# Kernel optimization log

Measured on AMD Instinct MI355X. Metric: run time of the kernel, lower is better.

Reference implementation:

```python
import jax, jax.numpy as jnp
import numpy as np

N, E, G, D = 100000, 1600000, 1000, 32
EPS = 1e-5


def setup_inputs() -> dict:
    key = jax.random.key(0)
    ks = jax.random.split(key, 24)
    inp = {
        'h': jax.random.normal(ks[0], (N, D), dtype=jnp.float32),
        'src': jax.random.randint(ks[1], (E,), 0, N, dtype=jnp.int32),
        'dst': jax.random.randint(ks[2], (E,), 0, N, dtype=jnp.int32),
        'graph_id': jnp.sort(jax.random.randint(ks[3], (N,), 0, G, dtype=jnp.int32)),
    }
    dims = [D, 32, 32, 32, 1]
    ki = 4
    for i in range(4):
        inp[f'conv_w{i}'] = jax.random.normal(ks[ki], (dims[i], dims[i + 1]), dtype=jnp.float32) * 0.1; ki += 1
        inp[f'conv_b{i}'] = jax.random.normal(ks[ki], (dims[i + 1],), dtype=jnp.float32) * 0.1; ki += 1
        inp[f'bn_g{i}'] = jnp.ones((dims[i + 1],), dtype=jnp.float32)
        inp[f'bn_b{i}'] = jnp.zeros((dims[i + 1],), dtype=jnp.float32)
    mlp_dims = [D + 32 + 32 + 32 + 1, 128, 64, 1]  # 129 -> 128 -> 64 -> 1
    for i in range(3):
        inp[f'mlp_w{i}'] = jax.random.normal(ks[ki], (mlp_dims[i], mlp_dims[i + 1]), dtype=jnp.float32) * 0.1; ki += 1
        inp[f'mlp_b{i}'] = jax.random.normal(ks[ki], (mlp_dims[i + 1],), dtype=jnp.float32) * 0.1; ki += 1
    return inp


def _mean_agg(x, src, dst):
    # DGL update_all(copy_u, mean): h'_v = mean of h_u over in-neighbors u of v
    deg = jax.ops.segment_sum(jnp.ones((src.shape[0],), x.dtype), dst, num_segments=N)
    agg = jax.ops.segment_sum(x[src], dst, num_segments=N)
    return agg / jnp.maximum(deg, 1.0)[:, None]


def _bn(x, g, b):
    # BatchNorm1d in training mode: batch statistics over node dim
    m = x.mean(axis=0)
    v = x.var(axis=0)
    return g * (x - m) * jax.lax.rsqrt(v + EPS) + b


def reference(h, src, dst, graph_id,
              conv_w0, conv_b0, conv_w1, conv_b1, conv_w2, conv_b2, conv_w3, conv_b3,
              bn_g0, bn_b0, bn_g1, bn_b1, bn_g2, bn_b2, bn_g3, bn_b3,
              mlp_w0, mlp_b0, mlp_w1, mlp_b1, mlp_w2, mlp_b2):
    conv = [(conv_w0, conv_b0), (conv_w1, conv_b1), (conv_w2, conv_b2), (conv_w3, conv_b3)]
    bn = [(bn_g0, bn_b0), (bn_g1, bn_b1), (bn_g2, bn_b2), (bn_g3, bn_b3)]
    h_list = [h]
    x = h
    for (w, b), (g, bb) in zip(conv, bn):
        x = _mean_agg(x, src, dst) @ w + b      # GCNConv
        x = jax.nn.relu(_bn(x, g, bb))           # BN + ReLU
        h_list.append(x)
    h_final = jnp.concatenate(h_list, axis=1)    # [N, 129]
    # dgl.mean_nodes: per-graph mean pool
    cnt = jax.ops.segment_sum(jnp.ones((N,), h_final.dtype), graph_id, num_segments=G)
    hg = jax.ops.segment_sum(h_final, graph_id, num_segments=G) / jnp.maximum(cnt, 1.0)[:, None]
    hg = jax.nn.relu(hg @ mlp_w0 + mlp_b0)
    hg = jax.nn.relu(hg @ mlp_w1 + mlp_b1)
    hg = hg @ mlp_w2 + mlp_b2
    return hg.reshape(-1)                         # [G]
```

## Files before the change

### kernel.cpp

```cpp
#include <hip/hip_runtime.h>

#define NSLOT 32
#define BN_EPS 1e-5f
#define NSB 256
#define BKBITS 8
#define BKN 256
#define MAXBUCK 512

static inline int cdiv_h(int a, int b) { return (a + b - 1) / b; }

__device__ __forceinline__ float4 f4add(float4 a, float4 b) {
    return make_float4(a.x + b.x, a.y + b.y, a.z + b.z, a.w + b.w);
}

__device__ __forceinline__ unsigned bf16rtn(float x) {
    unsigned u = __float_as_uint(x);
    return (u + 0x7FFFu + ((u >> 16) & 1u)) >> 16;
}
__device__ __forceinline__ unsigned bf16pack2(float lo, float hi) {
    return bf16rtn(lo) | (bf16rtn(hi) << 16);
}
__device__ __forceinline__ float bfLO(unsigned u) { return __uint_as_float(u << 16); }
__device__ __forceinline__ float bfHI(unsigned u) { return __uint_as_float(u & 0xFFFF0000u); }

__device__ __forceinline__ int blk_excl_scan256(int v, int t) {
    __shared__ int wsum[4];
    int l = t & 63, w = t >> 6;
    int incl = v;
#pragma unroll
    for (int off = 1; off < 64; off <<= 1) {
        int o = __shfl_up(incl, off, 64);
        if (l >= off) incl += o;
    }
    if (l == 63) wsum[w] = incl;
    __syncthreads();
    int wofs = 0;
#pragma unroll
    for (int i = 0; i < 4; i++) wofs += (i < w) ? wsum[i] : 0;
    __syncthreads();
    return wofs + incl - v;
}

__device__ __forceinline__ int blk_excl_scan512(int v, int t) {
    __shared__ int wsum8[8];
    int l = t & 63, w = t >> 6;
    int incl = v;
#pragma unroll
    for (int off = 1; off < 64; off <<= 1) {
        int o = __shfl_up(incl, off, 64);
        if (l >= off) incl += o;
    }
    if (l == 63) wsum8[w] = incl;
    __syncthreads();
    int wofs = 0;
#pragma unroll
    for (int i = 0; i < 8; i++) wofs += (i < w) ? wsum8[i] : 0;
    __syncthreads();
    return wofs + incl - v;
}

__device__ __forceinline__ void bn_coef(const float* __restrict__ sSum, const float* __restrict__ sSq,
                                        const float* __restrict__ bg, const float* __restrict__ bb,
                                        float invN, int ch, float* aOut, float* cOut) {
    float S = 0.f, Q = 0.f;
#pragma unroll
    for (int s = 0; s < NSLOT; s++) { S += sSum[s * 32 + ch]; Q += sSq[s * 32 + ch]; }
    float m = S * invN;
    float var = Q * invN - m * m;
    if (var < 0.f) var = 0.f;
    float iv = rsqrtf(var + BN_EPS);
    float a = bg[ch] * iv;
    *aOut = a;
    *cOut = bb[ch] - m * a;
}


__global__ __launch_bounds__(256) void k_hist(const int* __restrict__ dst, int* __restrict__ histT,
                                              float* __restrict__ sSum, float* __restrict__ sSq,
                                              int E, int nbuck, int chunk) {
    __shared__ int bins[MAXBUCK];
    int k = blockIdx.x, t = threadIdx.x;
    if (k == 0) {
        for (int i = t; i < 4 * NSLOT * 32; i += 256) { sSum[i] = 0.f; sSq[i] = 0.f; }
    }
    for (int b = t; b < nbuck; b += 256) bins[b] = 0;
    __syncthreads();
    int lo = k * chunk, hi = lo + chunk; if (hi > E) hi = E;
    for (int i = lo + t; i < hi; i += 256) atomicAdd(&bins[dst[i] >> BKBITS], 1);
    __syncthreads();
    for (int b = t; b < nbuck; b += 256) histT[k * nbuck + b] = bins[b];
}


__global__ __launch_bounds__(256) void k_scanA(const int* __restrict__ histT, int* __restrict__ prefixB,
                                               int* __restrict__ totalP, int* __restrict__ totalU,
                                               const int* __restrict__ gid, int* __restrict__ gstart,
                                               int nbuck, int N, int G) {
    int b = blockIdx.x, k = threadIdx.x;
    int i = b * 256 + k;
    if (i < N) {
        int g = gid[i];
        int gp = (i == 0) ? -1 : gid[i - 1];
        for (int x = gp + 1; x <= g; ++x) gstart[x] = i;
        if (i == N - 1) { for (int x = g + 1; x <= G; ++x) gstart[x] = N; }
    }
    int c = histT[k * nbuck + b];
    int pad = (c + 15) & ~15;
    int ep = blk_excl_scan256(pad, k);
    prefixB[b * NSB + k] = ep;
    int ec = blk_excl_scan256(c, k);
    if (k == NSB - 1) { totalP[b] = ep + pad; totalU[b] = ec + c; }
}

__global__ __launch_bounds__(512) void k_scanB(const int* __restrict__ totalP, const int* __restrict__ totalU,
                                               int* __restrict__ baseP, int* __restrict__ baseU, int nbuck) {
    int t = threadIdx.x;
    int vp = (t < nbuck) ? totalP[t] : 0;
    int vu = (t < nbuck) ? totalU[t] : 0;
    int ep = blk_excl_scan512(vp, t);
    int eu = blk_excl_scan512(vu, t);
    if (t < nbuck) { baseP[t] = ep; baseU[t] = eu; }
}


__global__ __launch_bounds__(256) void k_scatter2(const int* __restrict__ src, const int* __restrict__ dst,
                                                  const int* __restrict__ baseP, const int* __restrict__ prefixB,
                                                  unsigned* __restrict__ ebuf, int E, int nbuck, int chunk) {
    __shared__ int cur[MAXBUCK];
    int k = blockIdx.x, t = threadIdx.x;
    for (int b = t; b < nbuck; b += 256) cur[b] = baseP[b] + prefixB[b * NSB + k];
    __syncthreads();
    int lo = k * chunk, hi = lo + chunk; if (hi > E) hi = E;
    for (int i = lo + t; i < hi; i += 256) {
        int d = dst[i], s = src[i];
        int b = d >> BKBITS;
        int pos = atomicAdd(&cur[b], 1);
        ebuf[pos] = ((unsigned)(d & (BKN - 1)) << 24) | (unsigned)s;
    }
}


__global__ __launch_bounds__(256) void k_sortb(const unsigned* __restrict__ ebuf, const int* __restrict__ histT,
                                               const int* __restrict__ baseP, const int* __restrict__ prefixB,
                                               const int* __restrict__ baseU,
                                               int* __restrict__ col, int* __restrict__ rs, int* __restrict__ re,
                                               int nbuck, int N) {
    __shared__ int binCnt[BKN], binStart[BKN], cursor[BKN];
    __shared__ int cellBase[NSB], cellCnt[NSB];
    int b = blockIdx.x, t = threadIdx.x;
    cellBase[t] = baseP[b] + prefixB[b * NSB + t];
    cellCnt[t]  = histT[t * nbuck + b];
    binCnt[t] = 0; cursor[t] = 0;
    __syncthreads();
    {
        int cb = cellBase[t], cc = cellCnt[t];
        for (int j = 0; j < cc; j++) atomicAdd(&binCnt[ebuf[cb + j] >> 24], 1);
    }
    __syncthreads();
    int bs = blk_excl_scan256(binCnt[t], t);
    binStart[t] = bs;
    __syncthreads();
    int colBase = baseU[b];
    {
        int cb = cellBase[t], cc = cellCnt[t];
        for (int j = 0; j < cc; j++) {
            unsigned e = ebuf[cb + j];
            int l = e >> 24;
            int pos = binStart[l] + atomicAdd(&cursor[l], 1);
            col[colBase + pos] = (int)(e & 0xFFFFFFu);
        }
    }
    int node = b * BKN + t;
    if (node < N) {
        rs[node] = colBase + binStart[t];
        re[node] = colBase + binStart[t] + binCnt[t];
    }
}


template <int AFF>
__global__ __launch_bounds__(256) void k_transform(const void* __restrict__ xin, const float* __restrict__ W,
                                                   const float* __restrict__ sSum, const float* __restrict__ sSq,
                                                   const float* __restrict__ bg, const float* __restrict__ bb,
                                                   uint4* __restrict__ pb, int n, float invN) {
    __shared__ float sW[32][32];
    __shared__ float sA[32], sC[32];
    int t = threadIdx.x;
    for (int i = t; i < 1024; i += 256) sW[i >> 5][i & 31] = W[i];
    if (AFF && t < 32) bn_coef(sSum, sSq, bg, bb, invN, t, &sA[t], &sC[t]);
    __syncthreads();
    int node = blockIdx.x * 256 + t;
    if (node >= n) return;
    float x[32];
    if (AFF) {
        const uint4* y4 = (const uint4*)xin + (size_t)node * 4;
#pragma unroll
        for (int q = 0; q < 4; q++) {
            uint4 u = y4[q];
            x[8*q+0] = bfLO(u.x); x[8*q+1] = bfHI(u.x);
            x[8*q+2] = bfLO(u.y); x[8*q+3] = bfHI(u.y);
            x[8*q+4] = bfLO(u.z); x[8*q+5] = bfHI(u.z);
            x[8*q+6] = bfLO(u.w); x[8*q+7] = bfHI(u.w);
        }
#pragma unroll
        for (int k = 0; k < 32; k++) {
            float v = sA[k] * x[k] + sC[k];
            x[k] = v > 0.f ? v : 0.f;
        }
    } else {
        const float4* s4 = (const float4*)xin + (size_t)node * 8;
#pragma unroll
        for (int q = 0; q < 8; q++) {
            float4 v = s4[q];
            x[4*q] = v.x; x[4*q+1] = v.y; x[4*q+2] = v.z; x[4*q+3] = v.w;
        }
    }
    float acc[32];
#pragma unroll
    for (int f = 0; f < 32; f++) acc[f] = 0.f;
#pragma unroll
    for (int k = 0; k < 32; k++) {
        float xv = x[k];
#pragma unroll
        for (int f = 0; f < 32; f++) acc[f] += xv * sW[k][f];
    }
    uint4* d4 = pb + (size_t)node * 4;
#pragma unroll
    for (int q = 0; q < 4; q++) {
        uint4 o;
        o.x = bf16pack2(acc[8*q+0], acc[8*q+1]);
        o.y = bf16pack2(acc[8*q+2], acc[8*q+3]);
        o.z = bf16pack2(acc[8*q+4], acc[8*q+5]);
        o.w = bf16pack2(acc[8*q+6], acc[8*q+7]);
        d4[q] = o;
    }
}

__global__ __launch_bounds__(256) void k_transform3(const uint4* __restrict__ y2, const float* __restrict__ w3,
                                                    const float* __restrict__ sSum, const float* __restrict__ sSq,
                                                    const float* __restrict__ bg, const float* __restrict__ bb,
                                                    float* __restrict__ p3, int n, float invN) {
    __shared__ float sw[32], sA[32], sC[32];
    int t = threadIdx.x;
    if (t < 32) { sw[t] = w3[t]; bn_coef(sSum, sSq, bg, bb, invN, t, &sA[t], &sC[t]); }
    __syncthreads();
    int i = blockIdx.x * 256 + t;
    if (i >= n) return;
    const uint4* x4 = y2 + (size_t)i * 4;
    float acc = 0.f;
#pragma unroll
    for (int q = 0; q < 4; q++) {
        uint4 u = x4[q];
        float vv[8] = { bfLO(u.x), bfHI(u.x), bfLO(u.y), bfHI(u.y),
                        bfLO(u.z), bfHI(u.z), bfLO(u.w), bfHI(u.w) };
#pragma unroll
        for (int r = 0; r < 8; r++) {
            int k = q * 8 + r;
            float xv = sA[k] * vv[r] + sC[k];
            xv = xv > 0.f ? xv : 0.f;
            acc += xv * sw[k];
        }
    }
    p3[i] = acc;
}


__global__ __launch_bounds__(256, 6) void k_aggregate(const uint4* __restrict__ pb, const int* __restrict__ rs,
                                                      const int* __restrict__ re, const int* __restrict__ col,
                                                      const float* __restrict__ bias,
                                                      uint4* __restrict__ yb, float* __restrict__ sSum,
                                                      float* __restrict__ sSq, int n) {
    __shared__ int scol[2048];
    __shared__ float sWS[4][32];
    __shared__ float sWQ[4][32];
    int t = threadIdx.x;
    int lane = t & 3;
    int grp = t >> 2;
    int node0 = blockIdx.x * 64;
    int node = node0 + grp;
    int base0 = 0, len = 0;
    if (node0 < n) {
        int last = node0 + 63; if (last > n - 1) last = n - 1;
        base0 = rs[node0];
        len = re[last] - base0;
    }
    bool lds = (len > 0 && len <= 2048);
    if (lds) { for (int i = t; i < len; i += 256) scol[i] = col[base0 + i]; }
    __syncthreads();

    float accA[8], accB[8];
#pragma unroll
    for (int q = 0; q < 8; q++) { accA[q] = 0.f; accB[q] = 0.f; }
    float vout[8];
#pragma unroll
    for (int q = 0; q < 8; q++) vout[q] = 0.f;
    if (node < n) {
        int s0 = rs[node], s1 = re[node];
#define GATH2(vv, c) vv = pb[(size_t)(c) * 4 + lane]
#define ACC(dst, vv) \
        dst[0] += bfLO((vv).x); dst[1] += bfHI((vv).x); \
        dst[2] += bfLO((vv).y); dst[3] += bfHI((vv).y); \
        dst[4] += bfLO((vv).z); dst[5] += bfHI((vv).z); \
        dst[6] += bfLO((vv).w); dst[7] += bfHI((vv).w)
        if (lds) {
            int j = s0 - base0, j1 = s1 - base0;
            if (j + 4 <= j1) {
                uint4 g0, g1, g2, g3;
                GATH2(g0, scol[j]); GATH2(g1, scol[j + 1]); GATH2(g2, scol[j + 2]); GATH2(g3, scol[j + 3]);
                j += 4;
                for (; j + 4 <= j1; j += 4) {
                    uint4 h0, h1, h2, h3;
                    GATH2(h0, scol[j]); GATH2(h1, scol[j + 1]); GATH2(h2, scol[j + 2]); GATH2(h3, scol[j + 3]);
                    ACC(accA, g0); ACC(accB, g1); ACC(accA, g2); ACC(accB, g3);
                    g0 = h0; g1 = h1; g2 = h2; g3 = h3;
                }
                ACC(accA, g0); ACC(accB, g1); ACC(accA, g2); ACC(accB, g3);
            }
            for (; j < j1; ++j) { uint4 g; GATH2(g, scol[j]); ACC(accA, g); }
        } else {
            int j = s0;
            if (j + 4 <= s1) {
                uint4 g0, g1, g2, g3;
                GATH2(g0, col[j]); GATH2(g1, col[j + 1]); GATH2(g2, col[j + 2]); GATH2(g3, col[j + 3]);
                j += 4;
                for (; j + 4 <= s1; j += 4) {
                    uint4 h0, h1, h2, h3;
                    GATH2(h0, col[j]); GATH2(h1, col[j + 1]); GATH2(h2, col[j + 2]); GATH2(h3, col[j + 3]);
                    ACC(accA, g0); ACC(accB, g1); ACC(accA, g2); ACC(accB, g3);
                    g0 = h0; g1 = h1; g2 = h2; g3 = h3;
                }
                ACC(accA, g0); ACC(accB, g1); ACC(accA, g2); ACC(accB, g3);
            }
            for (; j < s1; ++j) { uint4 g; GATH2(g, col[j]); ACC(accA, g); }
        }
#undef GATH2
#undef ACC
        int deg = s1 - s0;
        float inv = (deg > 0) ? 1.f / (float)deg : 1.f;
        const float4* b4 = (const float4*)bias;
        float4 b0 = b4[lane * 2], b1 = b4[lane * 2 + 1];
        vout[0] = (accA[0] + accB[0]) * inv + b0.x;
        vout[1] = (accA[1] + accB[1]) * inv + b0.y;
        vout[2] = (accA[2] + accB[2]) * inv + b0.z;
        vout[3] = (accA[3] + accB[3]) * inv + b0.w;
        vout[4] = (accA[4] + accB[4]) * inv + b1.x;
        vout[5] = (accA[5] + accB[5]) * inv + b1.y;
        vout[6] = (accA[6] + accB[6]) * inv + b1.z;
        vout[7] = (accA[7] + accB[7]) * inv + b1.w;
        uint4 o;
        o.x = bf16pack2(vout[0], vout[1]);
        o.y = bf16pack2(vout[2], vout[3]);
        o.z = bf16pack2(vout[4], vout[5]);
        o.w = bf16pack2(vout[6], vout[7]);
        yb[(size_t)node * 4 + lane] = o;
    }
    float sqv[8];
#pragma unroll
    for (int q = 0; q < 8; q++) sqv[q] = vout[q] * vout[q];
#pragma unroll
    for (int off = 4; off < 64; off <<= 1) {
#pragma unroll
        for (int q = 0; q < 8; q++) {
            vout[q] += __shfl_xor(vout[q], off, 64);
            sqv[q]  += __shfl_xor(sqv[q],  off, 64);
        }
    }
    int w = t >> 6, l = t & 63;
    if (l < 4) {
#pragma unroll
        for (int q = 0; q < 8; q++) { sWS[w][l * 8 + q] = vout[q]; sWQ[w][l * 8 + q] = sqv[q]; }
    }
    __syncthreads();
    if (t < 32) {
        float S = sWS[0][t] + sWS[1][t] + sWS[2][t] + sWS[3][t];
        float Q = sWQ[0][t] + sWQ[1][t] + sWQ[2][t] + sWQ[3][t];
        int slot = blockIdx.x & (NSLOT - 1);
        atomicAdd(&sSum[slot * 32 + t], S);
        atomicAdd(&sSq[slot * 32 + t], Q);
    }
}

__global__ __launch_bounds__(256) void k_aggregate3(const float* __restrict__ p3, const int* __restrict__ rs,
                                                    const int* __restrict__ re, const int* __restrict__ col,
                                                    const float* __restrict__ b1,
                                                    float* __restrict__ y3, float* __restrict__ sSum,
                                                    float* __restrict__ sSq, int n) {
    int t = threadIdx.x;
    int i = blockIdx.x * 256 + t;
    float lsum = 0.f, lsq = 0.f;
    if (i < n) {
        int s0 = rs[i], s1 = re[i];
        float a0 = 0.f, a1 = 0.f, a2 = 0.f, a3 = 0.f;
        int j = s0;
        if (j + 4 <= s1) {
            float g0 = p3[col[j]], g1 = p3[col[j + 1]], g2 = p3[col[j + 2]], g3 = p3[col[j + 3]];
            j += 4;
            for (; j + 4 <= s1; j += 4) {
                float h0 = p3[col[j]], h1 = p3[col[j + 1]], h2 = p3[col[j + 2]], h3 = p3[col[j + 3]];
                a0 += g0; a1 += g1; a2 += g2; a3 += g3;
                g0 = h0; g1 = h1; g2 = h2; g3 = h3;
            }
            a0 += g0; a1 += g1; a2 += g2; a3 += g3;
        }
        for (; j < s1; ++j) a0 += p3[col[j]];
        float acc = (a0 + a1) + (a2 + a3);
        float inv = (s1 > s0) ? 1.f / (float)(s1 - s0) : 1.f;
        float v = acc * inv + b1[0];
        y3[i] = v; lsum = v; lsq = v * v;
    }
#pragma unroll
    for (int off = 1; off < 64; off <<= 1) {
        lsum += __shfl_xor(lsum, off, 64);
        lsq  += __shfl_xor(lsq,  off, 64);
    }
    __shared__ float sWS3[4], sWQ3[4];
    if ((t & 63) == 0) { sWS3[t >> 6] = lsum; sWQ3[t >> 6] = lsq; }
    __syncthreads();
    if (t == 0) {
        float S = sWS3[0] + sWS3[1] + sWS3[2] + sWS3[3];
        float Q = sWQ3[0] + sWQ3[1] + sWQ3[2] + sWQ3[3];
        int slot = blockIdx.x & (NSLOT - 1);
        atomicAdd(&sSum[slot * 32], S);
        atomicAdd(&sSq[slot * 32], Q);
    }
}


__global__ __launch_bounds__(256) void k_pool_mlp(const float* __restrict__ h,
                                                  const unsigned* __restrict__ y0b,
                                                  const unsigned* __restrict__ y1b,
                                                  const unsigned* __restrict__ y2b,
                                                  const float* __restrict__ y3,
                                                  const float* __restrict__ sSum, const float* __restrict__ sSq,
                                                  const float* __restrict__ bg0, const float* __restrict__ bb0,
                                                  const float* __restrict__ bg1, const float* __restrict__ bb1,
                                                  const float* __restrict__ bg2, const float* __restrict__ bb2,
                                                  const float* __restrict__ bg3, const float* __restrict__ bb3,
                                                  const int* __restrict__ gstart,
                                                  const float* __restrict__ w0, const float* __restrict__ b0,
                                                  const float* __restrict__ w1, const float* __restrict__ b1,
                                                  const float* __restrict__ w2, const float* __restrict__ b2,
                                                  float* __restrict__ out, float invN) {
    __shared__ float pcA[128], pcC[128];
    int g = blockIdx.x;
    int t = threadIdx.x;
    if (t < 97) {
        int layer = (t == 96) ? 3 : (t >> 5);
        int ch = t & 31;
        const float* bg = (layer == 0) ? bg0 : (layer == 1) ? bg1 : (layer == 2) ? bg2 : bg3;
        const float* bb = (layer == 0) ? bb0 : (layer == 1) ? bb1 : (layer == 2) ? bb2 : bb3;
        bn_coef(sSum + layer * NSLOT * 32, sSq + layer * NSLOT * 32, bg, bb, invN, ch, &pcA[t], &pcC[t]);
    }
    __syncthreads();
    int s0 = gstart[g], s1 = gstart[g + 1];
    int lane = t & 31, slot = t >> 5;
    int arr = lane >> 3, sub = lane & 7;
    const unsigned* yb = (arr == 1) ? y0b : (arr == 2) ? y1b : y2b;
    float4 a4 = make_float4(1.f, 1.f, 1.f, 1.f);
    float4 c4 = make_float4(0.f, 0.f, 0.f, 0.f);
    bool aff = (arr > 0);
    if (aff) {
        a4 = ((const float4*)pcA)[(arr - 1) * 8 + sub];
        c4 = ((const float4*)pcC)[(arr - 1) * 8 + sub];
    }
    float4 acc = make_float4(0.f, 0.f, 0.f, 0.f);
    for (int n = s0 + slot; n < s1; n += 8) {
        float4 v;
        if (arr == 0) {
            v = ((const float4*)h)[(size_t)n * 8 + sub];
        } else {
            uint2 u = ((const uint2*)yb)[(size_t)n * 8 + sub];
            v = make_float4(bfLO(u.x), bfHI(u.x), bfLO(u.y), bfHI(u.y));
        }
        if (aff) {
            float vx = fmaf(a4.x, v.x, c4.x); vx = vx > 0.f ? vx : 0.f;
            float vy = fmaf(a4.y, v.y, c4.y); vy = vy > 0.f ? vy : 0.f;
            float vz = fmaf(a4.z, v.z, c4.z); vz = vz > 0.f ? vz : 0.f;
            float vw = fmaf(a4.w, v.w, c4.w); vw = vw > 0.f ? vw : 0.f;
            v = make_float4(vx, vy, vz, vw);
        }
        acc = f4add(acc, v);
    }
    float ys = 0.f;
    {
        float a = pcA[96], c = pcC[96];
        for (int n = s0 + t; n < s1; n += 256) {
            float v = fmaf(a, y3[n], c);
            ys += v > 0.f ? v : 0.f;
        }
    }
#pragma unroll
    for (int off = 1; off < 64; off <<= 1) ys += __shfl_xor(ys, off, 64);
    __shared__ float sP[8][128];
    __shared__ float sY[4];
    if ((t & 63) == 0) sY[t >> 6] = ys;
    ((float4*)&sP[slot][lane * 4])[0] = acc;
    __syncthreads();
    __shared__ float hg[129];
    __shared__ float hid1[128];
    __shared__ float hid2[64];
    float inv = (s1 > s0) ? 1.f / (float)(s1 - s0) : 1.f;
    if (t < 128) {
        float S = 0.f;
#pragma unroll
        for (int s = 0; s < 8; s++) S += sP[s][t];
        hg[t] = S * inv;
    } else if (t == 128) {
        float S = sY[0] + sY[1] + sY[2] + sY[3];
        hg[128] = S * inv;
    }
    __syncthreads();
    if (t < 128) {
        float a = b0[t];
        for (int i = 0; i < 129; i++) a += hg[i] * w0[i * 128 + t];
        hid1[t] = a > 0.f ? a : 0.f;
    }
    __syncthreads();
    if (t < 64) {
        float a = b1[t];
        for (int i = 0; i < 128; i++) a += hid1[i] * w1[i * 64 + t];
        hid2[t] = a > 0.f ? a : 0.f;
    }
    __syncthreads();
    if (t < 64) {
        float v = hid2[t] * w2[t];
        for (int off = 32; off > 0; off >>= 1) v += __shfl_down(v, off, 64);
        if (t == 0) out[g] = v + b2[0];
    }
}


extern "C" void kernel_launch(void* const* d_in, const int* in_sizes, int n_in,
                              void* d_out, int out_size, void* d_ws, size_t ws_size,
                              hipStream_t stream) {
    const float* h   = (const float*)d_in[0];
    const int* src   = (const int*)d_in[1];
    const int* dst   = (const int*)d_in[2];
    const int* gid   = (const int*)d_in[3];
    const float* convw[4], *convb[4], *bng[4], *bnb[4];
    for (int i = 0; i < 4; i++) {
        convw[i] = (const float*)d_in[4 + 4 * i];
        convb[i] = (const float*)d_in[5 + 4 * i];
        bng[i]   = (const float*)d_in[6 + 4 * i];
        bnb[i]   = (const float*)d_in[7 + 4 * i];
    }
    const float* mw0 = (const float*)d_in[20];
    const float* mb0 = (const float*)d_in[21];
    const float* mw1 = (const float*)d_in[22];
    const float* mb1 = (const float*)d_in[23];
    const float* mw2 = (const float*)d_in[24];
    const float* mb2 = (const float*)d_in[25];

    const int N = in_sizes[0] / 32;
    const int E = in_sizes[1];
    const int G = out_size;
    const int nbuck = cdiv_h(N, BKN);
    const int chunk = cdiv_h(E, NSB);

    char* ws = (char*)d_ws;
    size_t off = 0;
    auto alloc = [&](size_t bytes) -> void* {
        void* p = ws + off;
        off += (bytes + 511) & ~(size_t)511;
        return p;
    };
    int* histT   = (int*)alloc((size_t)NSB * nbuck * 4);
    int* prefixB = (int*)alloc((size_t)nbuck * NSB * 4);
    int* totalP  = (int*)alloc((size_t)nbuck * 4);
    int* totalU  = (int*)alloc((size_t)nbuck * 4);
    int* basePp  = (int*)alloc((size_t)nbuck * 4);
    int* baseUp  = (int*)alloc((size_t)nbuck * 4);
    size_t ebufE = (size_t)E + (size_t)16 * NSB * nbuck;
    size_t ovl   = ebufE * 4;
    size_t pB    = (size_t)N * 64;
    if (pB > ovl) ovl = pB;
    unsigned* ebuf = (unsigned*)alloc(ovl);
    uint4* pb    = (uint4*)ebuf;
    int* col     = (int*)alloc((size_t)E * 4);
    int* rs      = (int*)alloc((size_t)N * 4);
    int* re      = (int*)alloc((size_t)N * 4);
    int* gstart  = (int*)alloc((size_t)(G + 1) * 4);
    uint4* y0b   = (uint4*)alloc((size_t)N * 64);
    uint4* y1b   = (uint4*)alloc((size_t)N * 64);
    uint4* y2b   = (uint4*)alloc((size_t)N * 64);
    float* y3    = (float*)alloc((size_t)N * 4);
    float* sSum  = (float*)alloc((size_t)4 * NSLOT * 32 * 4);
    float* sSq   = (float*)alloc((size_t)4 * NSLOT * 32 * 4);
    (void)ws_size; (void)n_in;

    const int NB_N = cdiv_h(N, 256);
    const int NB_AG = cdiv_h(N, 64);
    const float invN = 1.f / (float)N;

    k_hist<<<NSB, 256, 0, stream>>>(dst, histT, sSum, sSq, E, nbuck, chunk);
    k_scanA<<<nbuck, 256, 0, stream>>>(histT, prefixB, totalP, totalU, gid, gstart, nbuck, N, G);
    k_scanB<<<1, 512, 0, stream>>>(totalP, totalU, basePp, baseUp, nbuck);
    k_scatter2<<<NSB, 256, 0, stream>>>(src, dst, basePp, prefixB, ebuf, E, nbuck, chunk);
    k_sortb<<<nbuck, 256, 0, stream>>>(ebuf, histT, basePp, prefixB, baseUp, col, rs, re, nbuck, N);

    k_transform<0><<<NB_N, 256, 0, stream>>>(h, convw[0], nullptr, nullptr, nullptr, nullptr, pb, N, invN);
    k_aggregate<<<NB_AG, 256, 0, stream>>>(pb, rs, re, col, convb[0], y0b,
                                           sSum + 0 * NSLOT * 32, sSq + 0 * NSLOT * 32, N);
    k_transform<1><<<NB_N, 256, 0, stream>>>(y0b, convw[1], sSum + 0 * NSLOT * 32, sSq + 0 * NSLOT * 32,
                                             bng[0], bnb[0], pb, N, invN);
    k_aggregate<<<NB_AG, 256, 0, stream>>>(pb, rs, re, col, convb[1], y1b,
                                           sSum + 1 * NSLOT * 32, sSq + 1 * NSLOT * 32, N);
    k_transform<1><<<NB_N, 256, 0, stream>>>(y1b, convw[2], sSum + 1 * NSLOT * 32, sSq + 1 * NSLOT * 32,
                                             bng[1], bnb[1], pb, N, invN);
    k_aggregate<<<NB_AG, 256, 0, stream>>>(pb, rs, re, col, convb[2], y2b,
                                           sSum + 2 * NSLOT * 32, sSq + 2 * NSLOT * 32, N);
    k_transform3<<<NB_N, 256, 0, stream>>>(y2b, convw[3], sSum + 2 * NSLOT * 32, sSq + 2 * NSLOT * 32,
                                           bng[2], bnb[2], (float*)pb, N, invN);
    k_aggregate3<<<NB_N, 256, 0, stream>>>((float*)pb, rs, re, col, convb[3], y3,
                                           sSum + 3 * NSLOT * 32, sSq + 3 * NSLOT * 32, N);

    k_pool_mlp<<<G, 256, 0, stream>>>(h, (const unsigned*)y0b, (const unsigned*)y1b, (const unsigned*)y2b,
                                      y3, sSum, sSq,
                                      bng[0], bnb[0], bng[1], bnb[1], bng[2], bnb[2], bng[3], bnb[3],
                                      gstart, mw0, mb0, mw1, mb1, mw2, mb2, (float*)d_out, invN);
}
```

Before: 306.7 us.

## Fuse layer transforms into aggregation, merge hist with first transform, inline scans

Layers 1-3 now gather the previous layer's raw bf16 output, apply BN+ReLU per neighbor, and do the 32x32 matmul after aggregation inside one kernel, using linearity of the mean. This removes the separate transform kernels and their intermediate buffers. The first transform runs in extra blocks of the histogram kernel, and the single-block scanB is replaced by recomputing the bucket scan inside the scatter and sort kernels. The cost is redundant BN+ReLU work per edge instead of per node, plus a repeated small scan in every block.

```diff
diff --git a/kernel.cpp b/kernel.cpp
--- a/kernel.cpp
+++ b/kernel.cpp
@@ -37,24 +37,6 @@
     int wofs = 0;
 #pragma unroll
     for (int i = 0; i < 4; i++) wofs += (i < w) ? wsum[i] : 0;
-    __syncthreads();
-    return wofs + incl - v;
-}
-
-__device__ __forceinline__ int blk_excl_scan512(int v, int t) {
-    __shared__ int wsum8[8];
-    int l = t & 63, w = t >> 6;
-    int incl = v;
-#pragma unroll
-    for (int off = 1; off < 64; off <<= 1) {
-        int o = __shfl_up(incl, off, 64);
-        if (l >= off) incl += o;
-    }
-    if (l == 63) wsum8[w] = incl;
-    __syncthreads();
-    int wofs = 0;
-#pragma unroll
-    for (int i = 0; i < 8; i++) wofs += (i < w) ? wsum8[i] : 0;
     __syncthreads();
     return wofs + incl - v;
 }
@@ -75,20 +57,57 @@
 }
 
 
-__global__ __launch_bounds__(256) void k_hist(const int* __restrict__ dst, int* __restrict__ histT,
-                                              float* __restrict__ sSum, float* __restrict__ sSq,
-                                              int E, int nbuck, int chunk) {
+__global__ __launch_bounds__(256) void k_hist_t0(const int* __restrict__ dst, int* __restrict__ histT,
+                                                 float* __restrict__ sSum, float* __restrict__ sSq,
+                                                 int E, int nbuck, int chunk,
+                                                 const float* __restrict__ h, const float* __restrict__ W0,
+                                                 uint4* __restrict__ pb, int N) {
     __shared__ int bins[MAXBUCK];
-    int k = blockIdx.x, t = threadIdx.x;
-    if (k == 0) {
-        for (int i = t; i < 4 * NSLOT * 32; i += 256) { sSum[i] = 0.f; sSq[i] = 0.f; }
-    }
-    for (int b = t; b < nbuck; b += 256) bins[b] = 0;
-    __syncthreads();
-    int lo = k * chunk, hi = lo + chunk; if (hi > E) hi = E;
-    for (int i = lo + t; i < hi; i += 256) atomicAdd(&bins[dst[i] >> BKBITS], 1);
-    __syncthreads();
-    for (int b = t; b < nbuck; b += 256) histT[k * nbuck + b] = bins[b];
+    __shared__ float sW[32][32];
+    int t = threadIdx.x;
+    if (blockIdx.x < NSB) {
+        int k = blockIdx.x;
+        if (k == 0) {
+            for (int i = t; i < 4 * NSLOT * 32; i += 256) { sSum[i] = 0.f; sSq[i] = 0.f; }
+        }
+        for (int b = t; b < nbuck; b += 256) bins[b] = 0;
+        __syncthreads();
+        int lo = k * chunk, hi = lo + chunk; if (hi > E) hi = E;
+        for (int i = lo + t; i < hi; i += 256) atomicAdd(&bins[dst[i] >> BKBITS], 1);
+        __syncthreads();
+        for (int b = t; b < nbuck; b += 256) histT[k * nbuck + b] = bins[b];
+    } else {
+        for (int i = t; i < 1024; i += 256) sW[i >> 5][i & 31] = W0[i];
+        __syncthreads();
+        int node = (blockIdx.x - NSB) * 256 + t;
+        if (node >= N) return;
+        float x[32];
+        const float4* s4 = (const float4*)h + (size_t)node * 8;
+#pragma unroll
+        for (int q = 0; q < 8; q++) {
+            float4 v = s4[q];
+            x[4*q] = v.x; x[4*q+1] = v.y; x[4*q+2] = v.z; x[4*q+3] = v.w;
+        }
+        float acc[32];
+#pragma unroll
+        for (int f = 0; f < 32; f++) acc[f] = 0.f;
+#pragma unroll
+        for (int k = 0; k < 32; k++) {
+            float xv = x[k];
+#pragma unroll
+            for (int f = 0; f < 32; f++) acc[f] += xv * sW[k][f];
+        }
+        uint4* d4 = pb + (size_t)node * 4;
+#pragma unroll
+        for (int q = 0; q < 4; q++) {
+            uint4 o;
+            o.x = bf16pack2(acc[8*q+0], acc[8*q+1]);
+            o.y = bf16pack2(acc[8*q+2], acc[8*q+3]);
+            o.z = bf16pack2(acc[8*q+4], acc[8*q+5]);
+            o.w = bf16pack2(acc[8*q+6], acc[8*q+7]);
+            d4[q] = o;
+        }
+    }
 }
 
 
@@ -112,23 +131,29 @@
     if (k == NSB - 1) { totalP[b] = ep + pad; totalU[b] = ec + c; }
 }
 
-__global__ __launch_bounds__(512) void k_scanB(const int* __restrict__ totalP, const int* __restrict__ totalU,
-                                               int* __restrict__ baseP, int* __restrict__ baseU, int nbuck) {
-    int t = threadIdx.x;
-    int vp = (t < nbuck) ? totalP[t] : 0;
-    int vu = (t < nbuck) ? totalU[t] : 0;
-    int ep = blk_excl_scan512(vp, t);
-    int eu = blk_excl_scan512(vu, t);
-    if (t < nbuck) { baseP[t] = ep; baseU[t] = eu; }
+__device__ __forceinline__ void inline_scan512(const int* __restrict__ tot, int* __restrict__ sOut,
+                                               int* __restrict__ sTot, int nbuck, int t) {
+    int v0 = (t < nbuck) ? tot[t] : 0;
+    int v1 = (256 + t < nbuck) ? tot[256 + t] : 0;
+    int e0 = blk_excl_scan256(v0, t);
+    if (t == 255) *sTot = e0 + v0;
+    __syncthreads();
+    int e1 = blk_excl_scan256(v1, t) + *sTot;
+    sOut[t] = e0;
+    sOut[256 + t] = e1;
+    __syncthreads();
 }
 
 
 __global__ __launch_bounds__(256) void k_scatter2(const int* __restrict__ src, const int* __restrict__ dst,
-                                                  const int* __restrict__ baseP, const int* __restrict__ prefixB,
+                                                  const int* __restrict__ totalP, const int* __restrict__ prefixB,
                                                   unsigned* __restrict__ ebuf, int E, int nbuck, int chunk) {
     __shared__ int cur[MAXBUCK];
+    __shared__ int sBP[512];
+    __shared__ int sTot;
     int k = blockIdx.x, t = threadIdx.x;
-    for (int b = t; b < nbuck; b += 256) cur[b] = baseP[b] + prefixB[b * NSB + k];
+    inline_scan512(totalP, sBP, &sTot, nbuck, t);
+    for (int b = t; b < nbuck; b += 256) cur[b] = sBP[b] + prefixB[b * NSB + k];
     __syncthreads();
     int lo = k * chunk, hi = lo + chunk; if (hi > E) hi = E;
     for (int i = lo + t; i < hi; i += 256) {
@@ -141,14 +166,21 @@
 
 
 __global__ __launch_bounds__(256) void k_sortb(const unsigned* __restrict__ ebuf, const int* __restrict__ histT,
-                                               const int* __restrict__ baseP, const int* __restrict__ prefixB,
-                                               const int* __restrict__ baseU,
+                                               const int* __restrict__ totalP, const int* __restrict__ totalU,
+                                               const int* __restrict__ prefixB,
                                                int* __restrict__ col, int* __restrict__ rs, int* __restrict__ re,
                                                int nbuck, int N) {
     __shared__ int binCnt[BKN], binStart[BKN], cursor[BKN];
     __shared__ int cellBase[NSB], cellCnt[NSB];
+    __shared__ int sBP[512];
+    __shared__ int sTotS;
     int b = blockIdx.x, t = threadIdx.x;
-    cellBase[t] = baseP[b] + prefixB[b * NSB + t];
+    inline_scan512(totalP, sBP, &sTotS, nbuck, t);
+    int basePb = sBP[b];
+    __syncthreads();
+    inline_scan512(totalU, sBP, &sTotS, nbuck, t);
+    int baseUb = sBP[b];
+    cellBase[t] = basePb + prefixB[b * NSB + t];
     cellCnt[t]  = histT[t * nbuck + b];
     binCnt[t] = 0; cursor[t] = 0;
     __syncthreads();
@@ -160,108 +192,20 @@
     int bs = blk_excl_scan256(binCnt[t], t);
     binStart[t] = bs;
     __syncthreads();
-    int colBase = baseU[b];
     {
         int cb = cellBase[t], cc = cellCnt[t];
         for (int j = 0; j < cc; j++) {
             unsigned e = ebuf[cb + j];
             int l = e >> 24;
             int pos = binStart[l] + atomicAdd(&cursor[l], 1);
-            col[colBase + pos] = (int)(e & 0xFFFFFFu);
+            col[baseUb + pos] = (int)(e & 0xFFFFFFu);
         }
     }
     int node = b * BKN + t;
     if (node < N) {
-        rs[node] = colBase + binStart[t];
-        re[node] = colBase + binStart[t] + binCnt[t];
-    }
-}
-
-
-template <int AFF>
-__global__ __launch_bounds__(256) void k_transform(const void* __restrict__ xin, const float* __restrict__ W,
-                                                   const float* __restrict__ sSum, const float* __restrict__ sSq,
-                                                   const float* __restrict__ bg, const float* __restrict__ bb,
-                                                   uint4* __restrict__ pb, int n, float invN) {
-    __shared__ float sW[32][32];
-    __shared__ float sA[32], sC[32];
-    int t = threadIdx.x;
-    for (int i = t; i < 1024; i += 256) sW[i >> 5][i & 31] = W[i];
-    if (AFF && t < 32) bn_coef(sSum, sSq, bg, bb, invN, t, &sA[t], &sC[t]);
-    __syncthreads();
-    int node = blockIdx.x * 256 + t;
-    if (node >= n) return;
-    float x[32];
-    if (AFF) {
-        const uint4* y4 = (const uint4*)xin + (size_t)node * 4;
-#pragma unroll
-        for (int q = 0; q < 4; q++) {
-            uint4 u = y4[q];
-            x[8*q+0] = bfLO(u.x); x[8*q+1] = bfHI(u.x);
-            x[8*q+2] = bfLO(u.y); x[8*q+3] = bfHI(u.y);
-            x[8*q+4] = bfLO(u.z); x[8*q+5] = bfHI(u.z);
-            x[8*q+6] = bfLO(u.w); x[8*q+7] = bfHI(u.w);
-        }
-#pragma unroll
-        for (int k = 0; k < 32; k++) {
-            float v = sA[k] * x[k] + sC[k];
-            x[k] = v > 0.f ? v : 0.f;
-        }
-    } else {
-        const float4* s4 = (const float4*)xin + (size_t)node * 8;
-#pragma unroll
-        for (int q = 0; q < 8; q++) {
-            float4 v = s4[q];
-            x[4*q] = v.x; x[4*q+1] = v.y; x[4*q+2] = v.z; x[4*q+3] = v.w;
-        }
-    }
-    float acc[32];
-#pragma unroll
-    for (int f = 0; f < 32; f++) acc[f] = 0.f;
-#pragma unroll
-    for (int k = 0; k < 32; k++) {
-        float xv = x[k];
-#pragma unroll
-        for (int f = 0; f < 32; f++) acc[f] += xv * sW[k][f];
-    }
-    uint4* d4 = pb + (size_t)node * 4;
-#pragma unroll
-    for (int q = 0; q < 4; q++) {
-        uint4 o;
-        o.x = bf16pack2(acc[8*q+0], acc[8*q+1]);
-        o.y = bf16pack2(acc[8*q+2], acc[8*q+3]);
-        o.z = bf16pack2(acc[8*q+4], acc[8*q+5]);
-        o.w = bf16pack2(acc[8*q+6], acc[8*q+7]);
-        d4[q] = o;
-    }
-}
-
-__global__ __launch_bounds__(256) void k_transform3(const uint4* __restrict__ y2, const float* __restrict__ w3,
-                                                    const float* __restrict__ sSum, const float* __restrict__ sSq,
-                                                    const float* __restrict__ bg, const float* __restrict__ bb,
-                                                    float* __restrict__ p3, int n, float invN) {
-    __shared__ float sw[32], sA[32], sC[32];
-    int t = threadIdx.x;
-    if (t < 32) { sw[t] = w3[t]; bn_coef(sSum, sSq, bg, bb, invN, t, &sA[t], &sC[t]); }
-    __syncthreads();
-    int i = blockIdx.x * 256 + t;
-    if (i >= n) return;
-    const uint4* x4 = y2 + (size_t)i * 4;
-    float acc = 0.f;
-#pragma unroll
-    for (int q = 0; q < 4; q++) {
-        uint4 u = x4[q];
-        float vv[8] = { bfLO(u.x), bfHI(u.x), bfLO(u.y), bfHI(u.y),
-                        bfLO(u.z), bfHI(u.z), bfLO(u.w), bfHI(u.w) };
-#pragma unroll
-        for (int r = 0; r < 8; r++) {
-            int k = q * 8 + r;
-            float xv = sA[k] * vv[r] + sC[k];
-            xv = xv > 0.f ? xv : 0.f;
-            acc += xv * sw[k];
-        }
-    }
-    p3[i] = acc;
+        rs[node] = baseUb + binStart[t];
+        re[node] = baseUb + binStart[t] + binCnt[t];
+    }
 }
 
 
@@ -380,41 +324,236 @@
     }
 }
 
-__global__ __launch_bounds__(256) void k_aggregate3(const float* __restrict__ p3, const int* __restrict__ rs,
-                                                    const int* __restrict__ re, const int* __restrict__ col,
-                                                    const float* __restrict__ b1,
-                                                    float* __restrict__ y3, float* __restrict__ sSum,
-                                                    float* __restrict__ sSq, int n) {
+
+__global__ __launch_bounds__(256, 4) void k_aggF(const uint4* __restrict__ yin, const int* __restrict__ rs,
+                                                 const int* __restrict__ re, const int* __restrict__ col,
+                                                 const float* __restrict__ W, const float* __restrict__ bias,
+                                                 const float* __restrict__ pSum, const float* __restrict__ pSq,
+                                                 const float* __restrict__ bg, const float* __restrict__ bb,
+                                                 uint4* __restrict__ yout, float* __restrict__ sSum,
+                                                 float* __restrict__ sSq, int n, float invN) {
+    __shared__ int scol[2112];
+    __shared__ float sW[32][32];
+    __shared__ float sA[32], sC[32];
+    __shared__ float sWS[4][32];
+    __shared__ float sWQ[4][32];
+    float* sM = (float*)scol;
     int t = threadIdx.x;
-    int i = blockIdx.x * 256 + t;
-    float lsum = 0.f, lsq = 0.f;
-    if (i < n) {
-        int s0 = rs[i], s1 = re[i];
-        float a0 = 0.f, a1 = 0.f, a2 = 0.f, a3 = 0.f;
-        int j = s0;
-        if (j + 4 <= s1) {
-            float g0 = p3[col[j]], g1 = p3[col[j + 1]], g2 = p3[col[j + 2]], g3 = p3[col[j + 3]];
-            j += 4;
-            for (; j + 4 <= s1; j += 4) {
-                float h0 = p3[col[j]], h1 = p3[col[j + 1]], h2 = p3[col[j + 2]], h3 = p3[col[j + 3]];
-                a0 += g0; a1 += g1; a2 += g2; a3 += g3;
-                g0 = h0; g1 = h1; g2 = h2; g3 = h3;
+    for (int i = t; i < 1024; i += 256) sW[i >> 5][i & 31] = W[i];
+    if (t < 32) bn_coef(pSum, pSq, bg, bb, invN, t, &sA[t], &sC[t]);
+    int lane = t & 3, grp = t >> 2;
+    int node0 = blockIdx.x * 64, node = node0 + grp;
+    int base0 = 0, len = 0;
+    if (node0 < n) {
+        int last = node0 + 63; if (last > n - 1) last = n - 1;
+        base0 = rs[node0];
+        len = re[last] - base0;
+    }
+    bool lds = (len > 0 && len <= 2048);
+    __syncthreads();
+    if (lds) { for (int i = t; i < len; i += 256) scol[i] = col[base0 + i]; }
+    __syncthreads();
+    float a8[8], c8[8];
+#pragma unroll
+    for (int q = 0; q < 8; q++) { a8[q] = sA[lane * 8 + q]; c8[q] = sC[lane * 8 + q]; }
+
+    float accA[8], accB[8];
+#pragma unroll
+    for (int q = 0; q < 8; q++) { accA[q] = 0.f; accB[q] = 0.f; }
+    int s0 = 0, s1 = 0;
+    if (node < n) {
+        s0 = rs[node]; s1 = re[node];
+#define GATH2(vv, c) vv = yin[(size_t)(c) * 4 + lane]
+#define ACCF(dst, vv) do { \
+        float x0 = bfLO((vv).x), x1 = bfHI((vv).x), x2 = bfLO((vv).y), x3 = bfHI((vv).y); \
+        float x4 = bfLO((vv).z), x5 = bfHI((vv).z), x6 = bfLO((vv).w), x7 = bfHI((vv).w); \
+        float r0 = fmaf(a8[0], x0, c8[0]); dst[0] += r0 > 0.f ? r0 : 0.f; \
+        float r1 = fmaf(a8[1], x1, c8[1]); dst[1] += r1 > 0.f ? r1 : 0.f; \
+        float r2 = fmaf(a8[2], x2, c8[2]); dst[2] += r2 > 0.f ? r2 : 0.f; \
+        float r3 = fmaf(a8[3], x3, c8[3]); dst[3] += r3 > 0.f ? r3 : 0.f; \
+        float r4 = fmaf(a8[4], x4, c8[4]); dst[4] += r4 > 0.f ? r4 : 0.f; \
+        float r5 = fmaf(a8[5], x5, c8[5]); dst[5] += r5 > 0.f ? r5 : 0.f; \
+        float r6 = fmaf(a8[6], x6, c8[6]); dst[6] += r6 > 0.f ? r6 : 0.f; \
+        float r7 = fmaf(a8[7], x7, c8[7]); dst[7] += r7 > 0.f ? r7 : 0.f; } while (0)
+        if (lds) {
+            int j = s0 - base0, j1 = s1 - base0;
+            if (j + 4 <= j1) {
+                uint4 g0, g1, g2, g3;
+                GATH2(g0, scol[j]); GATH2(g1, scol[j + 1]); GATH2(g2, scol[j + 2]); GATH2(g3, scol[j + 3]);
+                j += 4;
+                for (; j + 4 <= j1; j += 4) {
+                    uint4 h0, h1, h2, h3;
+                    GATH2(h0, scol[j]); GATH2(h1, scol[j + 1]); GATH2(h2, scol[j + 2]); GATH2(h3, scol[j + 3]);
+                    ACCF(accA, g0); ACCF(accB, g1); ACCF(accA, g2); ACCF(accB, g3);
+                    g0 = h0; g1 = h1; g2 = h2; g3 = h3;
+                }
+                ACCF(accA, g0); ACCF(accB, g1); ACCF(accA, g2); ACCF(accB, g3);
             }
-            a0 += g0; a1 += g1; a2 += g2; a3 += g3;
-        }
-        for (; j < s1; ++j) a0 += p3[col[j]];
-        float acc = (a0 + a1) + (a2 + a3);
-        float inv = (s1 > s0) ? 1.f / (float)(s1 - s0) : 1.f;
-        float v = acc * inv + b1[0];
-        y3[i] = v; lsum = v; lsq = v * v;
-    }
+            for (; j < j1; ++j) { uint4 g; GATH2(g, scol[j]); ACCF(accA, g); }
+        } else {
+            int j = s0;
+            if (j + 4 <= s1) {
+                uint4 g0, g1, g2, g3;
+                GATH2(g0, col[j]); GATH2(g1, col[j + 1]); GATH2(g2, col[j + 2]); GATH2(g3, col[j + 3]);
+                j += 4;
+                for (; j + 4 <= s1; j += 4) {
+                    uint4 h0, h1, h2, h3;
+                    GATH2(h0, col[j]); GATH2(h1, col[j + 1]); GATH2(h2, col[j + 2]); GATH2(h3, col[j + 3]);
+                    ACCF(accA, g0); ACCF(accB, g1); ACCF(accA, g2); ACCF(accB, g3);
+                    g0 = h0; g1 = h1; g2 = h2; g3 = h3;
+                }
+                ACCF(accA, g0); ACCF(accB, g1); ACCF(accA, g2); ACCF(accB, g3);
+            }
+            for (; j < s1; ++j) { uint4 g; GATH2(g, col[j]); ACCF(accA, g); }
+        }
+#undef GATH2
+    }
+    __syncthreads();
+    if (node < n) {
+        int deg = s1 - s0;
+        float inv = (deg > 0) ? 1.f / (float)deg : 1.f;
+#pragma unroll
+        for (int q = 0; q < 8; q++) sM[grp * 33 + lane * 8 + q] = (accA[q] + accB[q]) * inv;
+    }
+    __syncthreads();
+    float vout[8];
+#pragma unroll
+    for (int q = 0; q < 8; q++) vout[q] = 0.f;
+    if (node < n) {
+        const float4* b4 = (const float4*)bias;
+        float4 b0 = b4[lane * 2], b1 = b4[lane * 2 + 1];
+        float out[8] = { b0.x, b0.y, b0.z, b0.w, b1.x, b1.y, b1.z, b1.w };
+#pragma unroll
+        for (int k = 0; k < 32; k++) {
+            float mk = sM[grp * 33 + k];
+#pragma unroll
+            for (int q = 0; q < 8; q++) out[q] += mk * sW[k][lane * 8 + q];
+        }
+#pragma unroll
+        for (int q = 0; q < 8; q++) vout[q] = out[q];
+        uint4 o;
+        o.x = bf16pack2(vout[0], vout[1]);
+        o.y = bf16pack2(vout[2], vout[3]);
+        o.z = bf16pack2(vout[4], vout[5]);
+        o.w = bf16pack2(vout[6], vout[7]);
+        yout[(size_t)node * 4 + lane] = o;
+    }
+    float sqv[8];
+#pragma unroll
+    for (int q = 0; q < 8; q++) sqv[q] = vout[q] * vout[q];
+#pragma unroll
+    for (int off = 4; off < 64; off <<= 1) {
+#pragma unroll
+        for (int q = 0; q < 8; q++) {
+            vout[q] += __shfl_xor(vout[q], off, 64);
+            sqv[q]  += __shfl_xor(sqv[q],  off, 64);
+        }
+    }
+    int w = t >> 6, l = t & 63;
+    if (l < 4) {
+#pragma unroll
+        for (int q = 0; q < 8; q++) { sWS[w][l * 8 + q] = vout[q]; sWQ[w][l * 8 + q] = sqv[q]; }
+    }
+    __syncthreads();
+    if (t < 32) {
+        float S = sWS[0][t] + sWS[1][t] + sWS[2][t] + sWS[3][t];
+        float Q = sWQ[0][t] + sWQ[1][t] + sWQ[2][t] + sWQ[3][t];
+        int slot = blockIdx.x & (NSLOT - 1);
+        atomicAdd(&sSum[slot * 32 + t], S);
+        atomicAdd(&sSq[slot * 32 + t], Q);
+    }
+}
+
+
+__global__ __launch_bounds__(256, 4) void k_aggF3(const uint4* __restrict__ yin, const int* __restrict__ rs,
+                                                  const int* __restrict__ re, const int* __restrict__ col,
+                                                  const float* __restrict__ w3, const float* __restrict__ b3,
+                                                  const float* __restrict__ pSum, const float* __restrict__ pSq,
+                                                  const float* __restrict__ bg, const float* __restrict__ bb,
+                                                  float* __restrict__ y3, float* __restrict__ sSum,
+                                                  float* __restrict__ sSq, int n, float invN) {
+    __shared__ int scol[2048];
+    __shared__ float sA[32], sC[32], sw[32];
+    __shared__ float sWS3[4], sWQ3[4];
+    int t = threadIdx.x;
+    if (t < 32) { sw[t] = w3[t]; bn_coef(pSum, pSq, bg, bb, invN, t, &sA[t], &sC[t]); }
+    int lane = t & 3, grp = t >> 2;
+    int node0 = blockIdx.x * 64, node = node0 + grp;
+    int base0 = 0, len = 0;
+    if (node0 < n) {
+        int last = node0 + 63; if (last > n - 1) last = n - 1;
+        base0 = rs[node0];
+        len = re[last] - base0;
+    }
+    bool lds = (len > 0 && len <= 2048);
+    __syncthreads();
+    if (lds) { for (int i = t; i < len; i += 256) scol[i] = col[base0 + i]; }
+    __syncthreads();
+    float a8[8], c8[8], w8[8];
+#pragma unroll
+    for (int q = 0; q < 8; q++) { a8[q] = sA[lane*8+q]; c8[q] = sC[lane*8+q]; w8[q] = sw[lane*8+q]; }
+
+    float accA[8], accB[8];
+#pragma unroll
+    for (int q = 0; q < 8; q++) { accA[q] = 0.f; accB[q] = 0.f; }
+    float yv = 0.f;
+    bool valid = (node < n);
+    if (valid) {
+        int s0 = rs[node], s1 = re[node];
+#define GATH2(vv, c) vv = yin[(size_t)(c) * 4 + lane]
+        if (lds) {
+            int j = s0 - base0, j1 = s1 - base0;
+            if (j + 4 <= j1) {
+                uint4 g0, g1, g2, g3;
+                GATH2(g0, scol[j]); GATH2(g1, scol[j + 1]); GATH2(g2, scol[j + 2]); GATH2(g3, scol[j + 3]);
+                j += 4;
+                for (; j + 4 <= j1; j += 4) {
+                    uint4 h0, h1, h2, h3;
+                    GATH2(h0, scol[j]); GATH2(h1, scol[j + 1]); GATH2(h2, scol[j + 2]); GATH2(h3, scol[j + 3]);
+                    ACCF(accA, g0); ACCF(accB, g1); ACCF(accA, g2); ACCF(accB, g3);
+                    g0 = h0; g1 = h1; g2 = h2; g3 = h3;
+                }
+                ACCF(accA, g0); ACCF(accB, g1); ACCF(accA, g2); ACCF(accB, g3);
+            }
+            for (; j < j1; ++j) { uint4 g; GATH2(g, scol[j]); ACCF(accA, g); }
+        } else {
+            int j = s0;
+            if (j + 4 <= s1) {
+                uint4 g0, g1, g2, g3;
+                GATH2(g0, col[j]); GATH2(g1, col[j + 1]); GATH2(g2, col[j + 2]); GATH2(g3, col[j + 3]);
+                j += 4;
+                for (; j + 4 <= s1; j += 4) {
+                    uint4 h0, h1, h2, h3;
+                    GATH2(h0, col[j]); GATH2(h1, col[j + 1]); GATH2(h2, col[j + 2]); GATH2(h3, col[j + 3]);
+                    ACCF(accA, g0); ACCF(accB, g1); ACCF(accA, g2); ACCF(accB, g3);
+                    g0 = h0; g1 = h1; g2 = h2; g3 = h3;
+                }
+                ACCF(accA, g0); ACCF(accB, g1); ACCF(accA, g2); ACCF(accB, g3);
+            }
+            for (; j < s1; ++j) { uint4 g; GATH2(g, col[j]); ACCF(accA, g); }
+        }
+#undef GATH2
+#undef ACCF
+        int deg = s1 - s0;
+        float inv = (deg > 0) ? 1.f / (float)deg : 1.f;
+        float part = 0.f;
+#pragma unroll
+        for (int q = 0; q < 8; q++) part += (accA[q] + accB[q]) * w8[q];
+        part *= inv;
+        part += __shfl_xor(part, 1, 64);
+        part += __shfl_xor(part, 2, 64);
+        yv = part + b3[0];
+        if (lane == 0) y3[node] = yv;
+    }
+    float sv = (valid && lane == 0) ? yv : 0.f;
+    float sq = sv * sv;
 #pragma unroll
     for (int off = 1; off < 64; off <<= 1) {
-        lsum += __shfl_xor(lsum, off, 64);
-        lsq  += __shfl_xor(lsq,  off, 64);
-    }
-    __shared__ float sWS3[4], sWQ3[4];
-    if ((t & 63) == 0) { sWS3[t >> 6] = lsum; sWQ3[t >> 6] = lsq; }
+        sv += __shfl_xor(sv, off, 64);
+        sq += __shfl_xor(sq, off, 64);
+    }
+    int w = t >> 6;
+    if ((t & 63) == 0) { sWS3[w] = sv; sWQ3[w] = sq; }
     __syncthreads();
     if (t == 0) {
         float S = sWS3[0] + sWS3[1] + sWS3[2] + sWS3[3];
@@ -568,14 +707,9 @@
     int* prefixB = (int*)alloc((size_t)nbuck * NSB * 4);
     int* totalP  = (int*)alloc((size_t)nbuck * 4);
     int* totalU  = (int*)alloc((size_t)nbuck * 4);
-    int* basePp  = (int*)alloc((size_t)nbuck * 4);
-    int* baseUp  = (int*)alloc((size_t)nbuck * 4);
     size_t ebufE = (size_t)E + (size_t)16 * NSB * nbuck;
-    size_t ovl   = ebufE * 4;
-    size_t pB    = (size_t)N * 64;
-    if (pB > ovl) ovl = pB;
-    unsigned* ebuf = (unsigned*)alloc(ovl);
-    uint4* pb    = (uint4*)ebuf;
+    unsigned* ebuf = (unsigned*)alloc(ebufE * 4);
+    uint4* pb    = (uint4*)alloc((size_t)N * 64);
     int* col     = (int*)alloc((size_t)E * 4);
     int* rs      = (int*)alloc((size_t)N * 4);
     int* re      = (int*)alloc((size_t)N * 4);
@@ -592,28 +726,22 @@
     const int NB_AG = cdiv_h(N, 64);
     const float invN = 1.f / (float)N;
 
-    k_hist<<<NSB, 256, 0, stream>>>(dst, histT, sSum, sSq, E, nbuck, chunk);
+    k_hist_t0<<<NSB + NB_N, 256, 0, stream>>>(dst, histT, sSum, sSq, E, nbuck, chunk,
+                                              h, convw[0], pb, N);
     k_scanA<<<nbuck, 256, 0, stream>>>(histT, prefixB, totalP, totalU, gid, gstart, nbuck, N, G);
-    k_scanB<<<1, 512, 0, stream>>>(totalP, totalU, basePp, baseUp, nbuck);
-    k_scatter2<<<NSB, 256, 0, stream>>>(src, dst, basePp, prefixB, ebuf, E, nbuck, chunk);
-    k_sortb<<<nbuck, 256, 0, stream>>>(ebuf, histT, basePp, prefixB, baseUp, col, rs, re, nbuck, N);
-
-    k_transform<0><<<NB_N, 256, 0, stream>>>(h, convw[0], nullptr, nullptr, nullptr, nullptr, pb, N, invN);
+    k_scatter2<<<NSB, 256, 0, stream>>>(src, dst, totalP, prefixB, ebuf, E, nbuck, chunk);
+    k_sortb<<<nbuck, 256, 0, stream>>>(ebuf, histT, totalP, totalU, prefixB, col, rs, re, nbuck, N);
     k_aggregate<<<NB_AG, 256, 0, stream>>>(pb, rs, re, col, convb[0], y0b,
                                            sSum + 0 * NSLOT * 32, sSq + 0 * NSLOT * 32, N);
-    k_transform<1><<<NB_N, 256, 0, stream>>>(y0b, convw[1], sSum + 0 * NSLOT * 32, sSq + 0 * NSLOT * 32,
-                                             bng[0], bnb[0], pb, N, invN);
-    k_aggregate<<<NB_AG, 256, 0, stream>>>(pb, rs, re, col, convb[1], y1b,
-                                           sSum + 1 * NSLOT * 32, sSq + 1 * NSLOT * 32, N);
-    k_transform<1><<<NB_N, 256, 0, stream>>>(y1b, convw[2], sSum + 1 * NSLOT * 32, sSq + 1 * NSLOT * 32,
-                                             bng[1], bnb[1], pb, N, invN);
-    k_aggregate<<<NB_AG, 256, 0, stream>>>(pb, rs, re, col, convb[2], y2b,
-                                           sSum + 2 * NSLOT * 32, sSq + 2 * NSLOT * 32, N);
-    k_transform3<<<NB_N, 256, 0, stream>>>(y2b, convw[3], sSum + 2 * NSLOT * 32, sSq + 2 * NSLOT * 32,
-                                           bng[2], bnb[2], (float*)pb, N, invN);
-    k_aggregate3<<<NB_N, 256, 0, stream>>>((float*)pb, rs, re, col, convb[3], y3,
-                                           sSum + 3 * NSLOT * 32, sSq + 3 * NSLOT * 32, N);
-
+    k_aggF<<<NB_AG, 256, 0, stream>>>(y0b, rs, re, col, convw[1], convb[1],
+                                      sSum + 0 * NSLOT * 32, sSq + 0 * NSLOT * 32, bng[0], bnb[0],
+                                      y1b, sSum + 1 * NSLOT * 32, sSq + 1 * NSLOT * 32, N, invN);
+    k_aggF<<<NB_AG, 256, 0, stream>>>(y1b, rs, re, col, convw[2], convb[2],
+                                      sSum + 1 * NSLOT * 32, sSq + 1 * NSLOT * 32, bng[1], bnb[1],
+                                      y2b, sSum + 2 * NSLOT * 32, sSq + 2 * NSLOT * 32, N, invN);
+    k_aggF3<<<NB_AG, 256, 0, stream>>>(y2b, rs, re, col, convw[3], convb[3],
+                                       sSum + 2 * NSLOT * 32, sSq + 2 * NSLOT * 32, bng[2], bnb[2],
+                                       y3, sSum + 3 * NSLOT * 32, sSq + 3 * NSLOT * 32, N, invN);
     k_pool_mlp<<<G, 256, 0, stream>>>(h, (const unsigned*)y0b, (const unsigned*)y1b, (const unsigned*)y2b,
                                       y3, sSum, sSq,
                                       bng[0], bnb[0], bng[1], bnb[1], bng[2], bnb[2], bng[3], bnb[3],
```

New measurement: 286.5 us. -6.6%, faster.
